# Kernel optimization log

Hardware: AMD Instinct MI355X
Metric: run time of the kernel (lower is better)

## Reference

```python
import jax, jax.numpy as jnp
import numpy as np


def setup_inputs() -> dict:
    key = jax.random.key(0)
    kq, kk, kv = jax.random.split(key, 3)
    B, N, M, H, D = 4, 2048, 2048, 8, 64
    queries = jax.random.normal(kq, (B, N, H, D), dtype=jnp.float32)
    keys = jax.random.normal(kk, (B, M, H, D), dtype=jnp.float32)
    values = jax.random.normal(kv, (B, M, H, D), dtype=jnp.float32)
    return {"queries": queries, "keys": keys, "values": values}


def reference(queries, keys, values):
    # queries: [B,N,H,D], keys/values: [B,M,H,D]
    D = queries.shape[3]
    softmax_temp = 1.0 / (D ** 0.5)
    QK = jnp.einsum('bnhd,bmhd->bnmh', queries, keys)  # [B,N,M,H]
    A = jax.nn.softmax(softmax_temp * QK, axis=2)      # softmax over M
    queried_values = jnp.einsum('bnmh,bmhd->bnhd', A, values)
    attention_weight = jnp.transpose(A, (0, 3, 1, 2))  # [B,H,N,M]
    return (queried_values, attention_weight)
```

## Files before the change

kernel.cpp:

```cpp
#include <hip/hip_runtime.h>

typedef __bf16 bf16x8 __attribute__((ext_vector_type(8)));
typedef float floatx4 __attribute__((ext_vector_type(4)));

#define MFMA(a, b, c) __builtin_amdgcn_mfma_f32_16x16x32_bf16((a), (b), (c), 0, 0, 0)

__device__ __forceinline__ unsigned short f2bf(float x) {
  union { float f; unsigned u; } v; v.f = x;
  unsigned r = v.u + 0x7FFFu + ((v.u >> 16) & 1u);
  return (unsigned short)(r >> 16);
}

constexpr int LD = 72;

__global__ __launch_bounds__(256, 4)
void attn_fwd(const float* __restrict__ Q, const float* __restrict__ K,
              const float* __restrict__ V, float* __restrict__ outQV,
              float* __restrict__ outA)
{
  __shared__ __align__(16) unsigned short Qs[64 * LD];
  __shared__ __align__(16) unsigned short Ks[64 * LD];
  __shared__ __align__(16) unsigned short Vts[64 * LD];
  __shared__ __align__(16) unsigned short As[64 * LD];

  const int tid = threadIdx.x;
  const int w  = tid >> 6;
  const int l  = tid & 63;
  const int c  = l & 15;
  const int q4 = l >> 4;

  const int bx = blockIdx.x;
  const int qt = bx & 31;
  const int h  = (bx >> 5) & 7;
  const int b  = bx >> 8;
  const int q0 = qt * 64;

  const float scale = 0.125f * 1.44269504088896340736f;

  const size_t base = (size_t)b * (2048 * 512) + (size_t)h * 64;
  const float* Qb = Q + base + (size_t)q0 * 512;
  const float* Kb = K + base;
  const float* Vb = V + base;

  const int r0 = tid >> 4;
  const int c4 = tid & 15;

  #pragma unroll
  for (int g = 0; g < 4; ++g) {
    int r = r0 + 16 * g;
    float4 qv = *(const float4*)(Qb + (size_t)r * 512 + c4 * 4);
    unsigned short* dst = &Qs[r * LD + c4 * 4];
    dst[0] = f2bf(qv.x * scale); dst[1] = f2bf(qv.y * scale);
    dst[2] = f2bf(qv.z * scale); dst[3] = f2bf(qv.w * scale);
  }

  float lsum[4] = {0.f, 0.f, 0.f, 0.f};
  for (int mc = 0; mc < 2048; mc += 64) {
    __syncthreads();
    #pragma unroll
    for (int g = 0; g < 4; ++g) {
      int r = r0 + 16 * g;
      float4 kv = *(const float4*)(Kb + (size_t)(mc + r) * 512 + c4 * 4);
      unsigned short* dst = &Ks[r * LD + c4 * 4];
      dst[0] = f2bf(kv.x); dst[1] = f2bf(kv.y);
      dst[2] = f2bf(kv.z); dst[3] = f2bf(kv.w);
    }
    __syncthreads();
    bf16x8 aQ0 = *(const bf16x8*)&Qs[(16 * w + c) * LD + q4 * 8];
    bf16x8 aQ1 = *(const bf16x8*)&Qs[(16 * w + c) * LD + 32 + q4 * 8];
    #pragma unroll
    for (int t = 0; t < 4; ++t) {
      bf16x8 bK0 = *(const bf16x8*)&Ks[(t * 16 + c) * LD + q4 * 8];
      bf16x8 bK1 = *(const bf16x8*)&Ks[(t * 16 + c) * LD + 32 + q4 * 8];
      floatx4 acc = {0.f, 0.f, 0.f, 0.f};
      acc = MFMA(aQ0, bK0, acc);
      acc = MFMA(aQ1, bK1, acc);
      #pragma unroll
      for (int i = 0; i < 4; ++i) lsum[i] += exp2f(acc[i]);
    }
  }
  float rcp[4];
  #pragma unroll
  for (int i = 0; i < 4; ++i) {
    float v = lsum[i];
    v += __shfl_xor(v, 1);
    v += __shfl_xor(v, 2);
    v += __shfl_xor(v, 4);
    v += __shfl_xor(v, 8);
    rcp[i] = 1.0f / v;
  }

  floatx4 Oacc[4];
  #pragma unroll
  for (int t = 0; t < 4; ++t) Oacc[t] = (floatx4){0.f, 0.f, 0.f, 0.f};

  float* aBase = outA + (((size_t)(b * 8 + h) * 2048 + q0 + 16 * w + q4 * 4) * 2048);

  for (int mc = 0; mc < 2048; mc += 64) {
    __syncthreads();
    #pragma unroll
    for (int g = 0; g < 4; ++g) {
      int r = r0 + 16 * g;
      float4 kv = *(const float4*)(Kb + (size_t)(mc + r) * 512 + c4 * 4);
      unsigned short* dst = &Ks[r * LD + c4 * 4];
      dst[0] = f2bf(kv.x); dst[1] = f2bf(kv.y);
      dst[2] = f2bf(kv.z); dst[3] = f2bf(kv.w);
    }
    #pragma unroll
    for (int g = 0; g < 4; ++g) {
      int m = r0 + 16 * g;
      float4 vv = *(const float4*)(Vb + (size_t)(mc + m) * 512 + c4 * 4);
      Vts[(c4 * 4 + 0) * LD + m] = f2bf(vv.x);
      Vts[(c4 * 4 + 1) * LD + m] = f2bf(vv.y);
      Vts[(c4 * 4 + 2) * LD + m] = f2bf(vv.z);
      Vts[(c4 * 4 + 3) * LD + m] = f2bf(vv.w);
    }
    __syncthreads();
    bf16x8 aQ0 = *(const bf16x8*)&Qs[(16 * w + c) * LD + q4 * 8];
    bf16x8 aQ1 = *(const bf16x8*)&Qs[(16 * w + c) * LD + 32 + q4 * 8];
    #pragma unroll
    for (int t = 0; t < 4; ++t) {
      bf16x8 bK0 = *(const bf16x8*)&Ks[(t * 16 + c) * LD + q4 * 8];
      bf16x8 bK1 = *(const bf16x8*)&Ks[(t * 16 + c) * LD + 32 + q4 * 8];
      floatx4 acc = {0.f, 0.f, 0.f, 0.f};
      acc = MFMA(aQ0, bK0, acc);
      acc = MFMA(aQ1, bK1, acc);
      #pragma unroll
      for (int i = 0; i < 4; ++i) {
        float a = exp2f(acc[i]) * rcp[i];
        aBase[(size_t)i * 2048 + mc + t * 16 + c] = a;
        As[(16 * w + q4 * 4 + i) * LD + t * 16 + c] = f2bf(a);
      }
    }
    bf16x8 aP0 = *(const bf16x8*)&As[(16 * w + c) * LD + q4 * 8];
    bf16x8 aP1 = *(const bf16x8*)&As[(16 * w + c) * LD + 32 + q4 * 8];
    #pragma unroll
    for (int t = 0; t < 4; ++t) {
      bf16x8 bV0 = *(const bf16x8*)&Vts[(t * 16 + c) * LD + q4 * 8];
      bf16x8 bV1 = *(const bf16x8*)&Vts[(t * 16 + c) * LD + 32 + q4 * 8];
      Oacc[t] = MFMA(aP0, bV0, Oacc[t]);
      Oacc[t] = MFMA(aP1, bV1, Oacc[t]);
    }
  }

  #pragma unroll
  for (int t = 0; t < 4; ++t) {
    #pragma unroll
    for (int i = 0; i < 4; ++i) {
      outQV[base + (size_t)(q0 + 16 * w + q4 * 4 + i) * 512 + t * 16 + c] = Oacc[t][i];
    }
  }
}

extern "C" void kernel_launch(void* const* d_in, const int* in_sizes, int n_in,
                              void* d_out, int out_size, void* d_ws, size_t ws_size,
                              hipStream_t stream)
{
  const float* Q = (const float*)d_in[0];
  const float* K = (const float*)d_in[1];
  const float* V = (const float*)d_in[2];
  float* outQV = (float*)d_out;
  float* outA  = (float*)d_out + 4194304;
  attn_fwd<<<dim3(1024), dim3(256), 0, stream>>>(Q, K, V, outQV, outA);
}
```

Measured before the change: 746.1 us.

## Transpose QK MFMA for vectorized attention stores and prefetch K/V into registers

Swaps the MFMA operand order so that each lane holds four consecutive key columns of one query row. This lets the attention-weight output be written as 16-byte nontemporal vector stores, and the bf16 probability tile be written to LDS as a vector. Q is kept in registers instead of LDS, and the next K/V tile is prefetched into registers during compute, which overlaps global loads with MFMA work. The row-sum reduction becomes a two-step cross-lane shuffle, and the fast exp2 intrinsic replaces exp2f. The cost is higher register pressure and an extra barrier per iteration.

After: 723.0 us. 3.1% less time.

```diff
diff --git a/kernel.cpp b/kernel.cpp
--- a/kernel.cpp
+++ b/kernel.cpp
@@ -2,6 +2,8 @@
 
 typedef __bf16 bf16x8 __attribute__((ext_vector_type(8)));
 typedef float floatx4 __attribute__((ext_vector_type(4)));
+typedef unsigned short ushort8 __attribute__((ext_vector_type(8)));
+typedef unsigned short ushort4v __attribute__((ext_vector_type(4)));
 
 #define MFMA(a, b, c) __builtin_amdgcn_mfma_f32_16x16x32_bf16((a), (b), (c), 0, 0, 0)
 
@@ -18,7 +20,6 @@
               const float* __restrict__ V, float* __restrict__ outQV,
               float* __restrict__ outA)
 {
-  __shared__ __align__(16) unsigned short Qs[64 * LD];
   __shared__ __align__(16) unsigned short Ks[64 * LD];
   __shared__ __align__(16) unsigned short Vts[64 * LD];
   __shared__ __align__(16) unsigned short As[64 * LD];
@@ -45,92 +46,106 @@
   const int r0 = tid >> 4;
   const int c4 = tid & 15;
 
+  bf16x8 bQ0, bQ1;
+  {
+    const float* qp = Qb + (size_t)(16 * w + c) * 512 + q4 * 8;
+    float4 qa0 = *(const float4*)(qp);
+    float4 qa1 = *(const float4*)(qp + 4);
+    float4 qb0 = *(const float4*)(qp + 32);
+    float4 qb1 = *(const float4*)(qp + 36);
+    ushort8 t0, t1;
+    t0[0]=f2bf(qa0.x*scale); t0[1]=f2bf(qa0.y*scale); t0[2]=f2bf(qa0.z*scale); t0[3]=f2bf(qa0.w*scale);
+    t0[4]=f2bf(qa1.x*scale); t0[5]=f2bf(qa1.y*scale); t0[6]=f2bf(qa1.z*scale); t0[7]=f2bf(qa1.w*scale);
+    t1[0]=f2bf(qb0.x*scale); t1[1]=f2bf(qb0.y*scale); t1[2]=f2bf(qb0.z*scale); t1[3]=f2bf(qb0.w*scale);
+    t1[4]=f2bf(qb1.x*scale); t1[5]=f2bf(qb1.y*scale); t1[6]=f2bf(qb1.z*scale); t1[7]=f2bf(qb1.w*scale);
+    bQ0 = __builtin_bit_cast(bf16x8, t0);
+    bQ1 = __builtin_bit_cast(bf16x8, t1);
+  }
+
+  float4 kreg[4];
   #pragma unroll
-  for (int g = 0; g < 4; ++g) {
-    int r = r0 + 16 * g;
-    float4 qv = *(const float4*)(Qb + (size_t)r * 512 + c4 * 4);
-    unsigned short* dst = &Qs[r * LD + c4 * 4];
-    dst[0] = f2bf(qv.x * scale); dst[1] = f2bf(qv.y * scale);
-    dst[2] = f2bf(qv.z * scale); dst[3] = f2bf(qv.w * scale);
-  }
+  for (int g = 0; g < 4; ++g)
+    kreg[g] = *(const float4*)(Kb + (size_t)(r0 + 16 * g) * 512 + c4 * 4);
 
   float lsum[4] = {0.f, 0.f, 0.f, 0.f};
   for (int mc = 0; mc < 2048; mc += 64) {
-    __syncthreads();
     #pragma unroll
     for (int g = 0; g < 4; ++g) {
-      int r = r0 + 16 * g;
-      float4 kv = *(const float4*)(Kb + (size_t)(mc + r) * 512 + c4 * 4);
-      unsigned short* dst = &Ks[r * LD + c4 * 4];
-      dst[0] = f2bf(kv.x); dst[1] = f2bf(kv.y);
-      dst[2] = f2bf(kv.z); dst[3] = f2bf(kv.w);
+      unsigned short* dst = &Ks[(r0 + 16 * g) * LD + c4 * 4];
+      dst[0] = f2bf(kreg[g].x); dst[1] = f2bf(kreg[g].y);
+      dst[2] = f2bf(kreg[g].z); dst[3] = f2bf(kreg[g].w);
     }
     __syncthreads();
-    bf16x8 aQ0 = *(const bf16x8*)&Qs[(16 * w + c) * LD + q4 * 8];
-    bf16x8 aQ1 = *(const bf16x8*)&Qs[(16 * w + c) * LD + 32 + q4 * 8];
+    if (mc + 64 < 2048) {
+      #pragma unroll
+      for (int g = 0; g < 4; ++g)
+        kreg[g] = *(const float4*)(Kb + (size_t)(mc + 64 + r0 + 16 * g) * 512 + c4 * 4);
+    }
     #pragma unroll
     for (int t = 0; t < 4; ++t) {
-      bf16x8 bK0 = *(const bf16x8*)&Ks[(t * 16 + c) * LD + q4 * 8];
-      bf16x8 bK1 = *(const bf16x8*)&Ks[(t * 16 + c) * LD + 32 + q4 * 8];
+      bf16x8 aK0 = *(const bf16x8*)&Ks[(t * 16 + c) * LD + q4 * 8];
+      bf16x8 aK1 = *(const bf16x8*)&Ks[(t * 16 + c) * LD + 32 + q4 * 8];
       floatx4 acc = {0.f, 0.f, 0.f, 0.f};
-      acc = MFMA(aQ0, bK0, acc);
-      acc = MFMA(aQ1, bK1, acc);
+      acc = MFMA(aK0, bQ0, acc);
+      acc = MFMA(aK1, bQ1, acc);
       #pragma unroll
-      for (int i = 0; i < 4; ++i) lsum[i] += exp2f(acc[i]);
+      for (int i = 0; i < 4; ++i) lsum[i] += __builtin_amdgcn_exp2f(acc[i]);
     }
+    __syncthreads();
   }
-  float rcp[4];
-  #pragma unroll
-  for (int i = 0; i < 4; ++i) {
-    float v = lsum[i];
-    v += __shfl_xor(v, 1);
-    v += __shfl_xor(v, 2);
-    v += __shfl_xor(v, 4);
-    v += __shfl_xor(v, 8);
-    rcp[i] = 1.0f / v;
-  }
+  float rs = (lsum[0] + lsum[1]) + (lsum[2] + lsum[3]);
+  rs += __shfl_xor(rs, 16);
+  rs += __shfl_xor(rs, 32);
+  const float rcp = 1.0f / rs;
 
   floatx4 Oacc[4];
   #pragma unroll
   for (int t = 0; t < 4; ++t) Oacc[t] = (floatx4){0.f, 0.f, 0.f, 0.f};
 
-  float* aBase = outA + (((size_t)(b * 8 + h) * 2048 + q0 + 16 * w + q4 * 4) * 2048);
+  float* aRowP = outA + (((size_t)(b * 8 + h) * 2048 + q0 + 16 * w + c) * 2048) + q4 * 4;
+
+  float4 vreg[4];
+  #pragma unroll
+  for (int g = 0; g < 4; ++g) {
+    kreg[g] = *(const float4*)(Kb + (size_t)(r0 + 16 * g) * 512 + c4 * 4);
+    vreg[g] = *(const float4*)(Vb + (size_t)(r0 + 16 * g) * 512 + c4 * 4);
+  }
 
   for (int mc = 0; mc < 2048; mc += 64) {
-    __syncthreads();
     #pragma unroll
     for (int g = 0; g < 4; ++g) {
-      int r = r0 + 16 * g;
-      float4 kv = *(const float4*)(Kb + (size_t)(mc + r) * 512 + c4 * 4);
-      unsigned short* dst = &Ks[r * LD + c4 * 4];
-      dst[0] = f2bf(kv.x); dst[1] = f2bf(kv.y);
-      dst[2] = f2bf(kv.z); dst[3] = f2bf(kv.w);
+      unsigned short* dst = &Ks[(r0 + 16 * g) * LD + c4 * 4];
+      dst[0] = f2bf(kreg[g].x); dst[1] = f2bf(kreg[g].y);
+      dst[2] = f2bf(kreg[g].z); dst[3] = f2bf(kreg[g].w);
+      int m = r0 + 16 * g;
+      Vts[(c4 * 4 + 0) * LD + m] = f2bf(vreg[g].x);
+      Vts[(c4 * 4 + 1) * LD + m] = f2bf(vreg[g].y);
+      Vts[(c4 * 4 + 2) * LD + m] = f2bf(vreg[g].z);
+      Vts[(c4 * 4 + 3) * LD + m] = f2bf(vreg[g].w);
+    }
+    __syncthreads();
+    if (mc + 64 < 2048) {
+      #pragma unroll
+      for (int g = 0; g < 4; ++g) {
+        kreg[g] = *(const float4*)(Kb + (size_t)(mc + 64 + r0 + 16 * g) * 512 + c4 * 4);
+        vreg[g] = *(const float4*)(Vb + (size_t)(mc + 64 + r0 + 16 * g) * 512 + c4 * 4);
+      }
     }
     #pragma unroll
-    for (int g = 0; g < 4; ++g) {
-      int m = r0 + 16 * g;
-      float4 vv = *(const float4*)(Vb + (size_t)(mc + m) * 512 + c4 * 4);
-      Vts[(c4 * 4 + 0) * LD + m] = f2bf(vv.x);
-      Vts[(c4 * 4 + 1) * LD + m] = f2bf(vv.y);
-      Vts[(c4 * 4 + 2) * LD + m] = f2bf(vv.z);
-      Vts[(c4 * 4 + 3) * LD + m] = f2bf(vv.w);
-    }
-    __syncthreads();
-    bf16x8 aQ0 = *(const bf16x8*)&Qs[(16 * w + c) * LD + q4 * 8];
-    bf16x8 aQ1 = *(const bf16x8*)&Qs[(16 * w + c) * LD + 32 + q4 * 8];
-    #pragma unroll
     for (int t = 0; t < 4; ++t) {
-      bf16x8 bK0 = *(const bf16x8*)&Ks[(t * 16 + c) * LD + q4 * 8];
-      bf16x8 bK1 = *(const bf16x8*)&Ks[(t * 16 + c) * LD + 32 + q4 * 8];
+      bf16x8 aK0 = *(const bf16x8*)&Ks[(t * 16 + c) * LD + q4 * 8];
+      bf16x8 aK1 = *(const bf16x8*)&Ks[(t * 16 + c) * LD + 32 + q4 * 8];
       floatx4 acc = {0.f, 0.f, 0.f, 0.f};
-      acc = MFMA(aQ0, bK0, acc);
-      acc = MFMA(aQ1, bK1, acc);
-      #pragma unroll
-      for (int i = 0; i < 4; ++i) {
-        float a = exp2f(acc[i]) * rcp[i];
-        aBase[(size_t)i * 2048 + mc + t * 16 + c] = a;
-        As[(16 * w + q4 * 4 + i) * LD + t * 16 + c] = f2bf(a);
-      }
+      acc = MFMA(aK0, bQ0, acc);
+      acc = MFMA(aK1, bQ1, acc);
+      floatx4 av;
+      av[0] = __builtin_amdgcn_exp2f(acc[0]) * rcp;
+      av[1] = __builtin_amdgcn_exp2f(acc[1]) * rcp;
+      av[2] = __builtin_amdgcn_exp2f(acc[2]) * rcp;
+      av[3] = __builtin_amdgcn_exp2f(acc[3]) * rcp;
+      __builtin_nontemporal_store(av, (floatx4*)(aRowP + mc + t * 16));
+      ushort4v us = { f2bf(av[0]), f2bf(av[1]), f2bf(av[2]), f2bf(av[3]) };
+      *(ushort4v*)&As[(16 * w + c) * LD + t * 16 + q4 * 4] = us;
     }
     bf16x8 aP0 = *(const bf16x8*)&As[(16 * w + c) * LD + q4 * 8];
     bf16x8 aP1 = *(const bf16x8*)&As[(16 * w + c) * LD + 32 + q4 * 8];
@@ -141,6 +156,7 @@
       Oacc[t] = MFMA(aP0, bV0, Oacc[t]);
       Oacc[t] = MFMA(aP1, bV1, Oacc[t]);
     }
+    __syncthreads();
   }
 
   #pragma unroll
```
